# Kernel optimization log

Measured on AMD Instinct MI355X. Metric: run time of the kernel, lower is better.

Reference implementation:

```python
import jax, jax.numpy as jnp
import numpy as np

D_MODEL = 2048
N_Q_HEADS = 32
N_KV_HEADS = 8
HEAD_DIM = D_MODEL // N_Q_HEADS  # 64
KV_DIM = HEAD_DIM * N_KV_HEADS   # 512
B, S = 2, 2048


def setup_inputs() -> dict:
    key = jax.random.key(0)
    ks = jax.random.split(key, 11)
    sc_d = 1.0 / np.sqrt(D_MODEL)
    return {
        "query": jax.random.normal(ks[0], (B, S, D_MODEL), jnp.float32),
        "key":   jax.random.normal(ks[1], (B, S, D_MODEL), jnp.float32),
        "value": jax.random.normal(ks[2], (B, S, D_MODEL), jnp.float32),
        "Wq": jax.random.normal(ks[3], (D_MODEL, D_MODEL), jnp.float32) * sc_d,
        "bq": jnp.zeros((D_MODEL,), jnp.float32),
        "Wk": jax.random.normal(ks[4], (D_MODEL, KV_DIM), jnp.float32) * sc_d,
        "bk": jnp.zeros((KV_DIM,), jnp.float32),
        "Wv": jax.random.normal(ks[5], (D_MODEL, KV_DIM), jnp.float32) * sc_d,
        "bv": jnp.zeros((KV_DIM,), jnp.float32),
        "Wo": jax.random.normal(ks[6], (D_MODEL, D_MODEL), jnp.float32) * sc_d,
        "bo": jnp.zeros((D_MODEL,), jnp.float32),
    }


def reference(query, key, value, Wq, bq, Wk, bk, Wv, bv, Wo, bo):
    b, s, _ = query.shape
    g = N_Q_HEADS // N_KV_HEADS  # num groups
    # projections
    Q = query @ Wq + bq                      # [b, s, d_model]
    K = key @ Wk + bk                        # [b, s, kv_dim]
    V = value @ Wv + bv                      # [b, s, kv_dim]
    # split heads. Torch code splits Q into groups of num_kv_heads heads,
    # and each group broadcasts per-head against the Hkv KV heads, i.e.
    # query head (grp*Hkv + j) attends against kv head j.
    Q = Q.reshape(b, s, g, N_KV_HEADS, HEAD_DIM)  # [b, s, g, hkv, d]
    K = K.reshape(b, s, N_KV_HEADS, HEAD_DIM)     # [b, s, hkv, d]
    V = V.reshape(b, s, N_KV_HEADS, HEAD_DIM)
    scale = 1.0 / jnp.sqrt(jnp.float32(HEAD_DIM))
    scores = jnp.einsum('bsghd,bthd->bghst', Q, K) * scale  # [b,g,hkv,s,s]
    attn = jax.nn.softmax(scores, axis=-1)
    out = jnp.einsum('bghst,bthd->bsghd', attn, V)          # [b,s,g,hkv,d]
    # concat over groups then heads == original head order (g major, hkv minor)
    out = out.reshape(b, s, D_MODEL)
    return out @ Wo + bo
```

## Files before the change

kernel.cpp:

```cpp
#include <hip/hip_runtime.h>
#include <cstdint>

typedef _Float16 half4 __attribute__((ext_vector_type(4)));
typedef _Float16 half8 __attribute__((ext_vector_type(8)));
typedef _Float16 half16 __attribute__((ext_vector_type(16)));
typedef float f32x4 __attribute__((ext_vector_type(4)));
typedef float f32x16 __attribute__((ext_vector_type(16)));

#define L2E 1.44269504088896340736f

__device__ __forceinline__ void gl16(const void* g, void* l) {
  __builtin_amdgcn_global_load_lds(
      (const __attribute__((address_space(1))) void*)g,
      (__attribute__((address_space(3))) void*)l, 16, 0, 0);
}

__device__ __forceinline__ uint32_t pk2(float a, float b) {
  return __builtin_bit_cast(uint32_t, __builtin_amdgcn_cvt_pkrtz(a, b));
}

__device__ __forceinline__ void plswap(uint32_t& x, uint32_t& y) {
  auto r = __builtin_amdgcn_permlane32_swap((int)x, (int)y, false, false);
  x = (uint32_t)r[0];
  y = (uint32_t)r[1];
}

__device__ __forceinline__ f32x16 zero16() {
  f32x16 z;
  #pragma unroll
  for (int r = 0; r < 16; ++r) z[r] = 0.0f;
  return z;
}

__global__ __launch_bounds__(256) void prep_all(
    const float* __restrict__ q, const float* __restrict__ k, const float* __restrict__ v,
    const float* __restrict__ Wq, const float* __restrict__ Wk,
    const float* __restrict__ Wv, const float* __restrict__ Wo,
    _Float16* __restrict__ qh, _Float16* __restrict__ kh, _Float16* __restrict__ vh,
    _Float16* __restrict__ WqkvT, _Float16* __restrict__ WoT)
{
  int id = blockIdx.x;
  const int tid = threadIdx.y * 32 + threadIdx.x;
  if (id < 12288) {
    const int z = id >> 12;
    const int x = id & 4095;
    const float* src = (z == 0) ? q : (z == 1 ? k : v);
    _Float16* dst    = (z == 0) ? qh : (z == 1 ? kh : vh);
    size_t i = ((size_t)x * 256 + tid) * 8;
    float4 a = *(const float4*)(src + i);
    float4 b = *(const float4*)(src + i + 4);
    half8 o;
    o[0] = (_Float16)a.x; o[1] = (_Float16)a.y; o[2] = (_Float16)a.z; o[3] = (_Float16)a.w;
    o[4] = (_Float16)b.x; o[5] = (_Float16)b.y; o[6] = (_Float16)b.z; o[7] = (_Float16)b.w;
    *(half8*)(dst + i) = o;
    return;
  }
  id -= 12288;
  const float* src;
  _Float16* dst;
  int N, tx, ty;
  if (id < 4096)      { src = Wq; dst = WqkvT;                        N = 2048; tx = id & 63; ty = id >> 6; }
  else if (id < 5120) { id -= 4096; src = Wk; dst = WqkvT + (size_t)2048 * 2048; N = 512; tx = id & 15; ty = id >> 4; }
  else if (id < 6144) { id -= 5120; src = Wv; dst = WqkvT + (size_t)2560 * 2048; N = 512; tx = id & 15; ty = id >> 4; }
  else                { id -= 6144; src = Wo; dst = WoT;              N = 2048; tx = id & 63; ty = id >> 6; }
  const int n0 = tx * 32, k0 = ty * 32;
  __shared__ float t[32][33];
  #pragma unroll
  for (int i = 0; i < 4; ++i)
    t[threadIdx.y + i * 8][threadIdx.x] =
        src[(size_t)(k0 + threadIdx.y + i * 8) * N + n0 + threadIdx.x];
  __syncthreads();
  #pragma unroll
  for (int i = 0; i < 4; ++i)
    dst[(size_t)(n0 + threadIdx.y + i * 8) * 2048 + k0 + threadIdx.x] =
        (_Float16)t[threadIdx.x][threadIdx.y + i * 8];
}

__global__ __launch_bounds__(256) void transpose_v(
    const _Float16* __restrict__ QKV, _Float16* __restrict__ VT)
{
  const int bh = blockIdx.z;
  const int bb = bh >> 3, h = bh & 7;
  const int t0 = blockIdx.x * 32, d0 = blockIdx.y * 32;
  __shared__ _Float16 t[32][33];
  const _Float16* src = QKV + (size_t)(bb * 2048) * 3072 + 2560 + h * 64;
  #pragma unroll
  for (int i = 0; i < 4; ++i)
    t[threadIdx.y + i * 8][threadIdx.x] =
        src[(size_t)(t0 + threadIdx.y + i * 8) * 3072 + d0 + threadIdx.x];
  __syncthreads();
  _Float16* dst = VT + ((size_t)(bb * 8 + h) * 64) * 2048;
  #pragma unroll
  for (int i = 0; i < 4; ++i)
    dst[(size_t)(d0 + threadIdx.y + i * 8) * 2048 + t0 + threadIdx.x] =
        t[threadIdx.x][threadIdx.y + i * 8];
}

template<int MODE>
__global__ __launch_bounds__(512, 2) void gemm128(
    const _Float16* __restrict__ Aq, const _Float16* __restrict__ Ak, const _Float16* __restrict__ Av,
    const _Float16* __restrict__ Bt,
    const float* __restrict__ bias0, const float* __restrict__ bias1, const float* __restrict__ bias2,
    _Float16* __restrict__ Ch, float* __restrict__ Cf)
{
  constexpr int K = 2048;
  constexpr int N = (MODE == 0) ? 3072 : 2048;
  constexpr int BN = (MODE == 0) ? 128 : 256;
  constexpr int NB = N / BN;
  constexpr int G = 32 * NB;
  constexpr int BUFB = BN * 64;
  constexpr int BUF = 8192 + BUFB;
  constexpr int NT = BN / 64;
  constexpr int NVM = 1 + BN / 128;

  const int wg = blockIdx.x;
  const int work = (wg & 7) * (G / 8) + (wg >> 3);
  const int m0 = (work / NB) * 128;
  const int n0 = (work % NB) * BN;

  const _Float16* A = Aq;
  if constexpr (MODE == 0) { if (n0 >= 2560) A = Av; else if (n0 >= 2048) A = Ak; }

  const int tid = threadIdx.x;
  const int lane = tid & 63;
  const int w = tid >> 6;
  const int wr = w >> 2;
  const int wc = w & 3;
  const int lo = lane & 15, hi = lane >> 4;

  __shared__ __align__(1024) char smem[3 * BUF];

  f32x4 acc[4][NT];
  #pragma unroll
  for (int mt = 0; mt < 4; ++mt)
    #pragma unroll
    for (int nt = 0; nt < NT; ++nt)
      acc[mt][nt] = (f32x4){0.f, 0.f, 0.f, 0.f};

  const _Float16* pB = Bt + (size_t)(n0 + w * (BN / 8) + (lane >> 2)) * K + (lane & 3) * 8;
  const _Float16* pA = A  + (size_t)(m0 + w * 16 + (lane >> 2)) * K + (lane & 3) * 8;
  const size_t bstep = (size_t)16 * K;
  const int dstB = 8192 + w * (BN / 8) * 64;
  const int dstA = w * 1024;

  #define STAGE(base)                                                         \
    do {                                                                      \
      gl16(pA, (base) + dstA);                                                \
      gl16(pB, (base) + dstB);                                                \
      if constexpr (MODE == 1) gl16(pB + bstep, (base) + dstB + 1024);        \
    } while (0)

  STAGE(smem);
  pA += 32; pB += 32;
  STAGE(smem + BUF);
  pA += 32; pB += 32;
  asm volatile("s_waitcnt vmcnt(%0)" :: "i"(NVM) : "memory");
  __builtin_amdgcn_s_barrier();

  const int abase = (wr * 64 + lo) * 64 + hi * 16;
  const int bbase = 8192 + (wc * (BN / 4) + lo) * 64 + hi * 16;

  int c = 0;
  for (int t = 0; t < 64; ++t) {
    int c1 = c + 1; if (c1 == 3) c1 = 0;
    int c2 = c1 + 1; if (c2 == 3) c2 = 0;
    if (t < 62) {
      STAGE(smem + c2 * BUF);
      pA += 32; pB += 32;
    }

    const char* bc = smem + c * BUF;
    half8 af[4], bf[NT];
    #pragma unroll
    for (int mt = 0; mt < 4; ++mt) af[mt] = *(const half8*)(bc + abase + mt * 1024);
    #pragma unroll
    for (int nt = 0; nt < NT; ++nt) bf[nt] = *(const half8*)(bc + bbase + nt * 1024);

    __builtin_amdgcn_s_setprio(1);
    #pragma unroll
    for (int mt = 0; mt < 4; ++mt)
      #pragma unroll
      for (int nt = 0; nt < NT; ++nt)
        acc[mt][nt] = __builtin_amdgcn_mfma_f32_16x16x32_f16(af[mt], bf[nt], acc[mt][nt], 0, 0, 0);
    __builtin_amdgcn_s_setprio(0);

    if (t < 62)       asm volatile("s_waitcnt vmcnt(%0)" :: "i"(NVM) : "memory");
    else if (t == 62) asm volatile("s_waitcnt vmcnt(0)" ::: "memory");
    if (t < 63) __builtin_amdgcn_s_barrier();
    c = c1;
  }
  #undef STAGE

  float* T = (float*)smem;
  const int tr = tid >> 4;
  const int sc = tid & 15;
  constexpr int CPS = BN / 16;
  #pragma unroll
  for (int mp = 0; mp < 4; ++mp) {
    __syncthreads();
    #pragma unroll
    for (int nt = 0; nt < NT; ++nt)
      #pragma unroll
      for (int r = 0; r < 4; ++r)
        T[(wr * 16 + 4 * hi + r) * BN + wc * (BN / 4) + nt * 16 + lo] = acc[mp][nt][r];
    __syncthreads();
    const int grow = m0 + (tr >> 4) * 64 + mp * 16 + (tr & 15);
    const int gcol = n0 + sc * CPS;
    const float* Trow = T + tr * BN + sc * CPS;
    const float* bp = bias0;
    int cb = gcol;
    if constexpr (MODE == 0) {
      if (gcol >= 2560) { bp = bias2; cb = gcol - 2560; }
      else if (gcol >= 2048) { bp = bias1; cb = gcol - 2048; }
    }
    if constexpr (MODE == 0) {
      float4 v0 = ((const float4*)Trow)[0];
      float4 v1 = ((const float4*)Trow)[1];
      float4 b0 = ((const float4*)(bp + cb))[0];
      float4 b1 = ((const float4*)(bp + cb))[1];
      half8 o;
      o[0] = (_Float16)(v0.x + b0.x); o[1] = (_Float16)(v0.y + b0.y);
      o[2] = (_Float16)(v0.z + b0.z); o[3] = (_Float16)(v0.w + b0.w);
      o[4] = (_Float16)(v1.x + b1.x); o[5] = (_Float16)(v1.y + b1.y);
      o[6] = (_Float16)(v1.z + b1.z); o[7] = (_Float16)(v1.w + b1.w);
      *(half8*)(Ch + (size_t)grow * N + gcol) = o;
    } else {
      float4 v[4];
      #pragma unroll
      for (int qq = 0; qq < 4; ++qq) v[qq] = ((const float4*)Trow)[qq];
      float4 bvv[4];
      #pragma unroll
      for (int qq = 0; qq < 4; ++qq) bvv[qq] = ((const float4*)(bp + cb))[qq];
      float* dstp = Cf + (size_t)grow * N + gcol;
      #pragma unroll
      for (int qq = 0; qq < 4; ++qq) {
        float4 ov = {v[qq].x + bvv[qq].x, v[qq].y + bvv[qq].y, v[qq].z + bvv[qq].z, v[qq].w + bvv[qq].w};
        ((float4*)dstp)[qq] = ov;
      }
    }
  }
}

__global__ __launch_bounds__(256, 4) void attn_fwd4(
    const _Float16* __restrict__ QKV, const _Float16* __restrict__ VT,
    _Float16* __restrict__ AO)
{
  const int wg = blockIdx.x;
  const int work = (wg & 7) * 128 + (wg >> 3);
  const int bh = work >> 6;
  const int b = bh >> 3, h = bh & 7;
  const int rem = work & 63;
  const int qh = (rem >> 4) * 8 + h;
  const int qt = rem & 15;

  const int tid = threadIdx.x;
  const int lane = tid & 63;
  const int w = tid >> 6;
  const int l31 = lane & 31;
  const int hi5 = lane >> 5;
  const int r7 = l31 & 7;

  __shared__ __align__(1024) char sm[2][2][8192];

  const _Float16 QSC = (_Float16)(0.125f * L2E);
  const int qrow0 = b * 2048 + qt * 128 + w * 32 + l31;
  half8 qf[4];
  {
    const _Float16* qp = QKV + (size_t)qrow0 * 3072 + qh * 64 + hi5 * 8;
    #pragma unroll
    for (int s = 0; s < 4; ++s) {
      half8 q = *(const half8*)(qp + s * 16);
      #pragma unroll
      for (int e = 0; e < 8; ++e) q[e] = q[e] * QSC;
      qf[s] = q;
    }
  }

  const int li = lane >> 3;
  const int lc = lane & 7;
  const int kslot = lc ^ li;
  const int w16li = w * 16 + li;
  const _Float16* Ksrc = QKV + ((size_t)(b * 2048 + w16li)) * 3072 + 2048 + h * 64 + kslot * 8;
  const _Float16* Vsrc = VT + ((size_t)(b * 8 + h) * 64 + w16li) * 2048 + kslot * 8;

  f32x16 oa[2];
  oa[0] = zero16();
  oa[1] = zero16();
  float lreg = 0.f;

  {
    char* kd = &sm[0][0][0] + w * 2048;
    char* vd = &sm[0][1][0] + w * 2048;
    gl16(Ksrc, kd);
    gl16(Ksrc + (size_t)8 * 3072, kd + 1024);
    gl16(Vsrc, vd);
    gl16(Vsrc + (size_t)8 * 2048, vd + 1024);
  }
  __syncthreads();

  int cur = 0;
  for (int t = 0; t < 32; ++t) {
    if (t < 31) {
      const int t0 = (t + 1) * 64;
      char* kd = &sm[cur ^ 1][0][0] + w * 2048;
      char* vd = &sm[cur ^ 1][1][0] + w * 2048;
      const _Float16* kg = Ksrc + (size_t)t0 * 3072;
      const _Float16* vg = Vsrc + t0;
      gl16(kg, kd);
      gl16(kg + (size_t)8 * 3072, kd + 1024);
      gl16(vg, vd);
      gl16(vg + (size_t)8 * 2048, vd + 1024);
    }

    const char* Kb = &sm[cur][0][0];
    const char* Vb = &sm[cur][1][0];

    uint32_t pw[4][4];
    float ps = 0.f;
    #pragma unroll
    for (int j = 0; j < 2; ++j) {
      f32x16 sa = zero16();
      const int kr = j * 32 + l31;
      __builtin_amdgcn_s_setprio(1);
      #pragma unroll
      for (int s = 0; s < 4; ++s) {
        half8 kf = *(const half8*)(Kb + kr * 128 + (((2 * s + hi5) ^ r7) << 4));
        sa = __builtin_amdgcn_mfma_f32_32x32x16_f16(kf, qf[s], sa, 0, 0, 0);
      }
      __builtin_amdgcn_s_setprio(0);
      #pragma unroll
      for (int r = 0; r < 16; ++r) {
        const float p = __builtin_amdgcn_exp2f(sa[r]);
        sa[r] = p;
        ps += p;
      }
      #pragma unroll
      for (int hf = 0; hf < 2; ++hf) {
        const int rb = hf * 8;
        uint32_t w0 = pk2(sa[rb + 0], sa[rb + 1]);
        uint32_t w1 = pk2(sa[rb + 2], sa[rb + 3]);
        uint32_t w2 = pk2(sa[rb + 4], sa[rb + 5]);
        uint32_t w3 = pk2(sa[rb + 6], sa[rb + 7]);
        plswap(w0, w2);
        plswap(w1, w3);
        const int s = 2 * j + hf;
        pw[s][0] = w0; pw[s][1] = w1; pw[s][2] = w2; pw[s][3] = w3;
      }
    }
    ps += __shfl_xor(ps, 32);
    lreg += ps;

    __builtin_amdgcn_s_setprio(1);
    #pragma unroll
    for (int s = 0; s < 4; ++s) {
      union { uint32_t u[4]; half8 h; } p0;
      #pragma unroll
      for (int u = 0; u < 4; ++u) p0.u[u] = pw[s][u];
      #pragma unroll
      for (int i = 0; i < 2; ++i) {
        const int vr = i * 32 + l31;
        half8 vf = *(const half8*)(Vb + vr * 128 + (((2 * s + hi5) ^ r7) << 4));
        oa[i] = __builtin_amdgcn_mfma_f32_32x32x16_f16(vf, p0.h, oa[i], 0, 0, 0);
      }
    }
    __builtin_amdgcn_s_setprio(0);

    __syncthreads();
    cur ^= 1;
  }

  {
    const float inv = 1.0f / lreg;
    #pragma unroll
    for (int i = 0; i < 2; ++i) {
      _Float16* dst = AO + (size_t)qrow0 * 2048 + qh * 64 + i * 32 + hi5 * 4;
      #pragma unroll
      for (int q = 0; q < 4; ++q) {
        union { uint32_t u[2]; half4 h4; } o;
        o.u[0] = pk2(oa[i][4 * q + 0] * inv, oa[i][4 * q + 1] * inv);
        o.u[1] = pk2(oa[i][4 * q + 2] * inv, oa[i][4 * q + 3] * inv);
        *(half4*)(dst + 8 * q) = o.h4;
      }
    }
  }
}

extern "C" void kernel_launch(void* const* d_in, const int* in_sizes, int n_in,
                              void* d_out, int out_size, void* d_ws, size_t ws_size,
                              hipStream_t stream) {
  const float* query = (const float*)d_in[0];
  const float* key   = (const float*)d_in[1];
  const float* value = (const float*)d_in[2];
  const float* Wq = (const float*)d_in[3];
  const float* bq = (const float*)d_in[4];
  const float* Wk = (const float*)d_in[5];
  const float* bk = (const float*)d_in[6];
  const float* Wv = (const float*)d_in[7];
  const float* bv = (const float*)d_in[8];
  const float* Wo = (const float*)d_in[9];
  const float* bo = (const float*)d_in[10];
  float* out = (float*)d_out;

  char* ws = (char*)d_ws;
  _Float16* qh    = (_Float16*)(ws);
  _Float16* kh    = (_Float16*)(ws + 16777216);
  _Float16* vh    = (_Float16*)(ws + 33554432);
  _Float16* WqkvT = (_Float16*)(ws + 50331648);
  _Float16* WoT   = (_Float16*)(ws + 62914560);
  _Float16* QKVh  = (_Float16*)(ws + 71303168);
  _Float16* VT    = (_Float16*)(ws + 96468992);
  _Float16* aoh   = (_Float16*)(ws + 100663296);

  prep_all<<<22528, dim3(32, 8), 0, stream>>>(query, key, value, Wq, Wk, Wv, Wo,
                                              qh, kh, vh, WqkvT, WoT);
  gemm128<0><<<768, 512, 0, stream>>>(qh, kh, vh, WqkvT, bq, bk, bv, QKVh, nullptr);
  transpose_v<<<dim3(64, 2, 16), dim3(32, 8), 0, stream>>>(QKVh, VT);
  attn_fwd4<<<1024, 256, 0, stream>>>(QKVh, VT, aoh);
  gemm128<1><<<256, 512, 0, stream>>>(aoh, nullptr, nullptr, WoT, bo,
                                      nullptr, nullptr, nullptr, out);
}
```

Measured before the change: 239.2 us.

## Fuse V transpose into QKV GEMM epilogue and shrink output GEMM tile

The V columns of the QKV projection are now written straight into the transposed VT layout from the GEMM epilogue, which removes the separate transpose_v kernel and its extra read and write of V. The output-projection GEMM drops from a 256-wide to a 128-wide N tile, so its grid doubles from 256 to 512 workgroups for better occupancy and CU coverage. The epilogue staging buffer gets a padded row stride of 136 to cut LDS bank conflicts. In exchange, the V epilogue makes strided LDS reads per thread, and the smaller output tile reuses A less.

```diff
diff --git a/kernel.cpp b/kernel.cpp
--- a/kernel.cpp
+++ b/kernel.cpp
@@ -76,47 +76,24 @@
         (_Float16)t[threadIdx.x][threadIdx.y + i * 8];
 }
 
-__global__ __launch_bounds__(256) void transpose_v(
-    const _Float16* __restrict__ QKV, _Float16* __restrict__ VT)
-{
-  const int bh = blockIdx.z;
-  const int bb = bh >> 3, h = bh & 7;
-  const int t0 = blockIdx.x * 32, d0 = blockIdx.y * 32;
-  __shared__ _Float16 t[32][33];
-  const _Float16* src = QKV + (size_t)(bb * 2048) * 3072 + 2560 + h * 64;
-  #pragma unroll
-  for (int i = 0; i < 4; ++i)
-    t[threadIdx.y + i * 8][threadIdx.x] =
-        src[(size_t)(t0 + threadIdx.y + i * 8) * 3072 + d0 + threadIdx.x];
-  __syncthreads();
-  _Float16* dst = VT + ((size_t)(bb * 8 + h) * 64) * 2048;
-  #pragma unroll
-  for (int i = 0; i < 4; ++i)
-    dst[(size_t)(d0 + threadIdx.y + i * 8) * 2048 + t0 + threadIdx.x] =
-        t[threadIdx.x][threadIdx.y + i * 8];
-}
-
 template<int MODE>
 __global__ __launch_bounds__(512, 2) void gemm128(
     const _Float16* __restrict__ Aq, const _Float16* __restrict__ Ak, const _Float16* __restrict__ Av,
     const _Float16* __restrict__ Bt,
     const float* __restrict__ bias0, const float* __restrict__ bias1, const float* __restrict__ bias2,
-    _Float16* __restrict__ Ch, float* __restrict__ Cf)
+    _Float16* __restrict__ Ch, float* __restrict__ Cf, _Float16* __restrict__ VTo)
 {
   constexpr int K = 2048;
   constexpr int N = (MODE == 0) ? 3072 : 2048;
-  constexpr int BN = (MODE == 0) ? 128 : 256;
-  constexpr int NB = N / BN;
+  constexpr int NB = N / 128;
   constexpr int G = 32 * NB;
-  constexpr int BUFB = BN * 64;
-  constexpr int BUF = 8192 + BUFB;
-  constexpr int NT = BN / 64;
-  constexpr int NVM = 1 + BN / 128;
+  constexpr int BUF = 8192 + 8192;
+  constexpr int TPAD = 136;
 
   const int wg = blockIdx.x;
   const int work = (wg & 7) * (G / 8) + (wg >> 3);
   const int m0 = (work / NB) * 128;
-  const int n0 = (work % NB) * BN;
+  const int n0 = (work % NB) * 128;
 
   const _Float16* A = Aq;
   if constexpr (MODE == 0) { if (n0 >= 2560) A = Av; else if (n0 >= 2048) A = Ak; }
@@ -130,35 +107,33 @@
 
   __shared__ __align__(1024) char smem[3 * BUF];
 
-  f32x4 acc[4][NT];
+  f32x4 acc[4][2];
   #pragma unroll
   for (int mt = 0; mt < 4; ++mt)
     #pragma unroll
-    for (int nt = 0; nt < NT; ++nt)
+    for (int nt = 0; nt < 2; ++nt)
       acc[mt][nt] = (f32x4){0.f, 0.f, 0.f, 0.f};
 
-  const _Float16* pB = Bt + (size_t)(n0 + w * (BN / 8) + (lane >> 2)) * K + (lane & 3) * 8;
+  const _Float16* pB = Bt + (size_t)(n0 + w * 16 + (lane >> 2)) * K + (lane & 3) * 8;
   const _Float16* pA = A  + (size_t)(m0 + w * 16 + (lane >> 2)) * K + (lane & 3) * 8;
-  const size_t bstep = (size_t)16 * K;
-  const int dstB = 8192 + w * (BN / 8) * 64;
+  const int dstB = 8192 + w * 1024;
   const int dstA = w * 1024;
 
   #define STAGE(base)                                                         \
     do {                                                                      \
       gl16(pA, (base) + dstA);                                                \
       gl16(pB, (base) + dstB);                                                \
-      if constexpr (MODE == 1) gl16(pB + bstep, (base) + dstB + 1024);        \
     } while (0)
 
   STAGE(smem);
   pA += 32; pB += 32;
   STAGE(smem + BUF);
   pA += 32; pB += 32;
-  asm volatile("s_waitcnt vmcnt(%0)" :: "i"(NVM) : "memory");
+  asm volatile("s_waitcnt vmcnt(2)" ::: "memory");
   __builtin_amdgcn_s_barrier();
 
   const int abase = (wr * 64 + lo) * 64 + hi * 16;
-  const int bbase = 8192 + (wc * (BN / 4) + lo) * 64 + hi * 16;
+  const int bbase = 8192 + (wc * 32 + lo) * 64 + hi * 16;
 
   int c = 0;
   for (int t = 0; t < 64; ++t) {
@@ -170,72 +145,82 @@
     }
 
     const char* bc = smem + c * BUF;
-    half8 af[4], bf[NT];
+    half8 af[4], bf[2];
     #pragma unroll
     for (int mt = 0; mt < 4; ++mt) af[mt] = *(const half8*)(bc + abase + mt * 1024);
     #pragma unroll
-    for (int nt = 0; nt < NT; ++nt) bf[nt] = *(const half8*)(bc + bbase + nt * 1024);
+    for (int nt = 0; nt < 2; ++nt) bf[nt] = *(const half8*)(bc + bbase + nt * 1024);
 
     __builtin_amdgcn_s_setprio(1);
     #pragma unroll
     for (int mt = 0; mt < 4; ++mt)
       #pragma unroll
-      for (int nt = 0; nt < NT; ++nt)
+      for (int nt = 0; nt < 2; ++nt)
         acc[mt][nt] = __builtin_amdgcn_mfma_f32_16x16x32_f16(af[mt], bf[nt], acc[mt][nt], 0, 0, 0);
     __builtin_amdgcn_s_setprio(0);
 
-    if (t < 62)       asm volatile("s_waitcnt vmcnt(%0)" :: "i"(NVM) : "memory");
+    if (t < 62)       asm volatile("s_waitcnt vmcnt(2)" ::: "memory");
     else if (t == 62) asm volatile("s_waitcnt vmcnt(0)" ::: "memory");
     if (t < 63) __builtin_amdgcn_s_barrier();
     c = c1;
   }
   #undef STAGE
 
+  const bool isV = (MODE == 0) && (n0 >= 2560);
   float* T = (float*)smem;
   const int tr = tid >> 4;
   const int sc = tid & 15;
-  constexpr int CPS = BN / 16;
   #pragma unroll
   for (int mp = 0; mp < 4; ++mp) {
     __syncthreads();
     #pragma unroll
-    for (int nt = 0; nt < NT; ++nt)
+    for (int nt = 0; nt < 2; ++nt)
       #pragma unroll
       for (int r = 0; r < 4; ++r)
-        T[(wr * 16 + 4 * hi + r) * BN + wc * (BN / 4) + nt * 16 + lo] = acc[mp][nt][r];
+        T[(wr * 16 + 4 * hi + r) * TPAD + wc * 32 + nt * 16 + lo] = acc[mp][nt][r];
     __syncthreads();
-    const int grow = m0 + (tr >> 4) * 64 + mp * 16 + (tr & 15);
-    const int gcol = n0 + sc * CPS;
-    const float* Trow = T + tr * BN + sc * CPS;
-    const float* bp = bias0;
-    int cb = gcol;
-    if constexpr (MODE == 0) {
-      if (gcol >= 2560) { bp = bias2; cb = gcol - 2560; }
-      else if (gcol >= 2048) { bp = bias1; cb = gcol - 2048; }
-    }
-    if constexpr (MODE == 0) {
+    if (isV) {
+      const int cv = tid & 127;
+      const int tg = tid >> 7;
+      const int run = tg >> 1, hb = tg & 1;
+      const int vd = n0 - 2560 + cv;
+      const int hV = vd >> 6, dV = vd & 63;
+      const float bias = bias2[vd];
+      const int trow0 = run * 16 + hb * 8;
+      const int tglob = m0 + run * 64 + mp * 16 + hb * 8;
+      const int bb = tglob >> 11;
+      const int tloc = tglob & 2047;
+      half8 o;
+      #pragma unroll
+      for (int e = 0; e < 8; ++e)
+        o[e] = (_Float16)(T[(trow0 + e) * TPAD + cv] + bias);
+      *(half8*)(VTo + ((size_t)(bb * 8 + hV) * 64 + dV) * 2048 + tloc) = o;
+    } else {
+      const int grow = m0 + (tr >> 4) * 64 + mp * 16 + (tr & 15);
+      const int gcol = n0 + sc * 8;
+      const float* Trow = T + tr * TPAD + sc * 8;
+      const float* bp = bias0;
+      int cb = gcol;
+      if constexpr (MODE == 0) {
+        if (gcol >= 2048) { bp = bias1; cb = gcol - 2048; }
+      }
       float4 v0 = ((const float4*)Trow)[0];
       float4 v1 = ((const float4*)Trow)[1];
       float4 b0 = ((const float4*)(bp + cb))[0];
       float4 b1 = ((const float4*)(bp + cb))[1];
-      half8 o;
-      o[0] = (_Float16)(v0.x + b0.x); o[1] = (_Float16)(v0.y + b0.y);
-      o[2] = (_Float16)(v0.z + b0.z); o[3] = (_Float16)(v0.w + b0.w);
-      o[4] = (_Float16)(v1.x + b1.x); o[5] = (_Float16)(v1.y + b1.y);
-      o[6] = (_Float16)(v1.z + b1.z); o[7] = (_Float16)(v1.w + b1.w);
-      *(half8*)(Ch + (size_t)grow * N + gcol) = o;
-    } else {
-      float4 v[4];
-      #pragma unroll
-      for (int qq = 0; qq < 4; ++qq) v[qq] = ((const float4*)Trow)[qq];
-      float4 bvv[4];
-      #pragma unroll
-      for (int qq = 0; qq < 4; ++qq) bvv[qq] = ((const float4*)(bp + cb))[qq];
-      float* dstp = Cf + (size_t)grow * N + gcol;
-      #pragma unroll
-      for (int qq = 0; qq < 4; ++qq) {
-        float4 ov = {v[qq].x + bvv[qq].x, v[qq].y + bvv[qq].y, v[qq].z + bvv[qq].z, v[qq].w + bvv[qq].w};
-        ((float4*)dstp)[qq] = ov;
+      if constexpr (MODE == 0) {
+        half8 o;
+        o[0] = (_Float16)(v0.x + b0.x); o[1] = (_Float16)(v0.y + b0.y);
+        o[2] = (_Float16)(v0.z + b0.z); o[3] = (_Float16)(v0.w + b0.w);
+        o[4] = (_Float16)(v1.x + b1.x); o[5] = (_Float16)(v1.y + b1.y);
+        o[6] = (_Float16)(v1.z + b1.z); o[7] = (_Float16)(v1.w + b1.w);
+        *(half8*)(Ch + (size_t)grow * N + gcol) = o;
+      } else {
+        float* dstp = Cf + (size_t)grow * N + gcol;
+        float4 o0 = {v0.x + b0.x, v0.y + b0.y, v0.z + b0.z, v0.w + b0.w};
+        float4 o1 = {v1.x + b1.x, v1.y + b1.y, v1.z + b1.z, v1.w + b1.w};
+        ((float4*)dstp)[0] = o0;
+        ((float4*)dstp)[1] = o1;
       }
     }
   }
@@ -413,9 +398,9 @@
 
   prep_all<<<22528, dim3(32, 8), 0, stream>>>(query, key, value, Wq, Wk, Wv, Wo,
                                               qh, kh, vh, WqkvT, WoT);
-  gemm128<0><<<768, 512, 0, stream>>>(qh, kh, vh, WqkvT, bq, bk, bv, QKVh, nullptr);
-  transpose_v<<<dim3(64, 2, 16), dim3(32, 8), 0, stream>>>(QKVh, VT);
+  gemm128<0><<<768, 512, 0, stream>>>(qh, kh, vh, WqkvT, bq, bk, bv,
+                                      QKVh, nullptr, VT);
   attn_fwd4<<<1024, 256, 0, stream>>>(QKVh, VT, aoh);
-  gemm128<1><<<256, 512, 0, stream>>>(aoh, nullptr, nullptr, WoT, bo,
-                                      nullptr, nullptr, nullptr, out);
-}
+  gemm128<1><<<512, 512, 0, stream>>>(aoh, nullptr, nullptr, WoT, bo,
+                                      nullptr, nullptr, nullptr, out, nullptr);
+}
```

Result: faster. 231.8 us, median of 2 (-3.1%).
